# Kernel optimization log

Measured on AMD Instinct MI355X. Metric: run time of the kernel, lower is better.

Reference implementation:

```python
import jax, jax.numpy as jnp
import numpy as np

N_NODES = 100000
N_EDGES = 3200000
D = 256
REPEAT = 2
FACTOR = 0.5


def setup_inputs() -> dict:
    key = jax.random.key(0)
    k1, k2, k3, k4, k5, k6 = jax.random.split(key, 6)
    x = jax.random.normal(k1, (N_NODES, D), dtype=jnp.float32)
    vals = jax.random.uniform(k2, (N_EDGES,), dtype=jnp.float32)
    # Xavier-ish scale for linear weights
    W0 = jax.random.normal(k3, (D, D), dtype=jnp.float32) / np.sqrt(D)
    W1 = jax.random.normal(k4, (D, D), dtype=jnp.float32) / np.sqrt(D)
    rows = jax.random.randint(k5, (N_EDGES,), 0, N_NODES, dtype=jnp.int32)
    cols = jax.random.randint(k6, (N_EDGES,), 0, N_NODES, dtype=jnp.int32)
    return {"x": x, "vals": vals, "W0": W0, "W1": W1, "rows": rows, "cols": cols}


def reference(x, vals, W0, W1, rows, cols):
    # support is sparse [N, N] in COO: support[rows[e], cols[e]] = vals[e]
    def spmm(h):
        # gather source-node features, scale by edge weight, scatter-add to dst
        return jax.ops.segment_sum(vals[:, None] * h[cols], rows,
                                   num_segments=N_NODES)

    h = x
    for W, act in ((W0, jax.nn.relu), (W1, lambda v: v)):
        # _propagate: repeated SpMM with scalar factor
        for _ in range(REPEAT):
            h = spmm(h) * FACTOR
        # linear (no bias) + activation
        h = act(h @ W)
    return h
```

## Files before the change

kernel.cpp:

```cpp
#include <hip/hip_runtime.h>
#include <hip/hip_bf16.h>
#include <hip/hip_fp16.h>

#define N_D 256
#define NBLK 832

typedef __attribute__((ext_vector_type(8))) short bf16x8;
typedef __attribute__((ext_vector_type(4))) float f32x4;

__device__ __forceinline__ unsigned short f2bf(float f) {
  union { float f; unsigned u; } c; c.f = f;
  unsigned u = c.u;
  return (unsigned short)((u + 0x7fffu + ((u >> 16) & 1u)) >> 16);
}
__device__ __forceinline__ float asf(unsigned u) {
  union { unsigned u; float f; } c; c.u = u;
  return c.f;
}
__device__ __forceinline__ int grp_of(int r, unsigned gmagic) {
  int g = (int)(((unsigned long long)(unsigned)r * gmagic) >> 37);
  return min(g, 7);
}

__global__ __launch_bounds__(256) void conv_kernel(
    const float* __restrict__ in, unsigned short* __restrict__ out, int n4) {
  int i = blockIdx.x * 256 + threadIdx.x;
  if (i < n4) {
    float4 v = reinterpret_cast<const float4*>(in)[i];
    ushort4 o;
    o.x = f2bf(v.x); o.y = f2bf(v.y); o.z = f2bf(v.z); o.w = f2bf(v.w);
    reinterpret_cast<ushort4*>(out)[i] = o;
  }
}

__global__ __launch_bounds__(256) void count_kernel(
    const int* __restrict__ rows, int* __restrict__ cnt, int* __restrict__ cntT,
    int n_edges, unsigned gmagic) {
  __shared__ int lcnt[8];
  if (threadIdx.x < 8) lcnt[threadIdx.x] = 0;
  __syncthreads();
  for (int e = blockIdx.x * 256 + threadIdx.x; e < n_edges; e += NBLK * 256) {
    const int r = rows[e];
    atomicAdd(&cnt[r], 1);
    atomicAdd(&lcnt[grp_of(r, gmagic)], 1);
  }
  __syncthreads();
  if (threadIdx.x < 8) cntT[threadIdx.x * NBLK + blockIdx.x] = lcnt[threadIdx.x];
}

__global__ __launch_bounds__(1024) void scan_kernel(
    const int* __restrict__ cnt, int* __restrict__ outA,
    int* __restrict__ outB, int n) {
  __shared__ int wsum[16];
  __shared__ int carry_sh;
  const int tid = threadIdx.x;
  const int lane = tid & 63;
  const int wid = tid >> 6;
  if (tid == 0) carry_sh = 0;
  __syncthreads();
  for (int base = 0; base < n; base += 4096) {
    const int i0 = base + tid * 4;
    int4 v = make_int4(0, 0, 0, 0);
    if (i0 + 3 < n) v = *reinterpret_cast<const int4*>(cnt + i0);
    else {
      if (i0     < n) v.x = cnt[i0];
      if (i0 + 1 < n) v.y = cnt[i0 + 1];
      if (i0 + 2 < n) v.z = cnt[i0 + 2];
    }
    const int s1 = v.x, s2 = s1 + v.y, s3 = s2 + v.z, s4 = s3 + v.w;
    int ws = s4;
#pragma unroll
    for (int off = 1; off < 64; off <<= 1) {
      int o = __shfl_up(ws, off, 64);
      if (lane >= off) ws += o;
    }
    if (lane == 63) wsum[wid] = ws;
    __syncthreads();
    if (wid == 0) {
      int t = (lane < 16) ? wsum[lane] : 0;
#pragma unroll
      for (int off = 1; off < 16; off <<= 1) {
        int o = __shfl_up(t, off, 64);
        if (lane >= off) t += o;
      }
      if (lane < 16) wsum[lane] = t;
    }
    __syncthreads();
    const int carry = carry_sh;
    const int tbase = carry + (wid ? wsum[wid - 1] : 0) + ws - s4;
    if (i0     < n) { outA[i0]     = tbase;      outB[i0]     = tbase; }
    if (i0 + 1 < n) { outA[i0 + 1] = tbase + s1; outB[i0 + 1] = tbase + s1; }
    if (i0 + 2 < n) { outA[i0 + 2] = tbase + s2; outB[i0 + 2] = tbase + s2; }
    if (i0 + 3 < n) { outA[i0 + 3] = tbase + s3; outB[i0 + 3] = tbase + s3; }
    __syncthreads();
    if (tid == 0) carry_sh = carry + wsum[15];
    __syncthreads();
  }
  if (tid == 0) outA[n] = carry_sh;
}

__global__ __launch_bounds__(256) void partition_kernel(
    const int* __restrict__ rows, const int* __restrict__ cols,
    const float* __restrict__ vals, const int* __restrict__ pofsT,
    int2* __restrict__ part, int n_edges, unsigned gmagic) {
  __shared__ int lofs[8];
  if (threadIdx.x < 8) lofs[threadIdx.x] = pofsT[threadIdx.x * NBLK + blockIdx.x];
  __syncthreads();
  for (int e = blockIdx.x * 256 + threadIdx.x; e < n_edges; e += NBLK * 256) {
    const int r = rows[e];
    const int g = grp_of(r, gmagic);
    const int slot = atomicAdd(&lofs[g], 1);
    const unsigned short hb = __half_as_ushort(__float2half_rn(vals[e] * 0.5f));
    int2 rv;
    rv.x = r;
    rv.y = (int)(((unsigned)cols[e] << 15) | ((unsigned)hb >> 1));
    part[slot] = rv;
  }
}

__global__ __launch_bounds__(256) void scatter2_kernel(
    const int2* __restrict__ part, const int* __restrict__ pofsT,
    int* __restrict__ cursor, unsigned* __restrict__ colpack) {
  const int g  = blockIdx.x & 7;
  const int bk = blockIdx.x >> 3;
  const int nb = gridDim.x >> 3;
  const int s0 = pofsT[g * NBLK];
  const int s1 = pofsT[(g + 1) * NBLK];
  for (int i = s0 + bk * 256 + threadIdx.x; i < s1; i += nb * 256) {
    const int2 rv = part[i];
    const int pos = atomicAdd(&cursor[rv.x], 1);
    colpack[pos] = (unsigned)rv.y;
  }
}

__global__ __launch_bounds__(256) void spmm_slice(
    const unsigned short* __restrict__ hin, const int* __restrict__ row_ptr,
    const unsigned* __restrict__ colpack, unsigned short* __restrict__ hout,
    int n_nodes) {
  const int slice = blockIdx.x & 3;
  const int lane = threadIdx.x & 63;
  const int half = lane >> 5;
  const int sub  = lane & 31;
  const int wgid = ((blockIdx.x >> 2) * 256 + threadIdx.x) >> 6;
  const int node = wgid * 2 + half;
  const bool ok = node < n_nodes;
  int start = 0, end = 0;
  if (ok) { start = row_ptr[node]; end = row_ptr[node + 1]; }

  const unsigned* __restrict__ hinw = reinterpret_cast<const unsigned*>(hin);
  const int fofs = slice * 32 + sub;

  float acc0 = 0.f, acc1 = 0.f;

  for (int base = start; base < end; base += 32) {
    const int cnt = min(32, end - base);
    unsigned u = 0;
    if (base + sub < end) u = colpack[base + sub];
    for (int t = 0; t < cnt; t += 8) {
      unsigned hv[8];
      float v[8];
#pragma unroll
      for (int j = 0; j < 8; ++j) {
        const unsigned ue = (unsigned)__shfl((int)u, (half << 5) + t + j, 64);
        const int c = (int)(ue >> 15);
        v[j] = __half2float(__ushort_as_half((unsigned short)((ue & 0x7fffu) << 1)));
        hv[j] = hinw[(size_t)c * 128 + fofs];
      }
#pragma unroll
      for (int j = 0; j < 8; ++j) {
        acc0 += v[j] * asf(hv[j] << 16);
        acc1 += v[j] * asf(hv[j] & 0xffff0000u);
      }
    }
  }
  if (ok) {
    reinterpret_cast<unsigned*>(hout)[(size_t)node * 128 + fofs] =
        (unsigned)f2bf(acc0) | ((unsigned)f2bf(acc1) << 16);
  }
}

__global__ __launch_bounds__(256) void wconv_kernel(
    const float* __restrict__ W, unsigned short* __restrict__ WT) {
  int k = blockIdx.x;
  int n = threadIdx.x;
  WT[(size_t)n * N_D + k] = f2bf(W[(size_t)k * N_D + n]);
}

template <bool RELU, bool OUT_BF16>
__global__ __launch_bounds__(256) void gemm_csr(
    const unsigned short* __restrict__ H, const unsigned short* __restrict__ WT,
    void* __restrict__ C, int M) {
  const int wave = threadIdx.x >> 6;
  const int lane = threadIdx.x & 63;
  const int m = lane & 15;
  const int p = lane >> 4;
  const int row0 = blockIdx.x * 64;
  const int col0 = wave * 64;

  f32x4 acc[4][4];
#pragma unroll
  for (int i = 0; i < 4; ++i)
#pragma unroll
    for (int j = 0; j < 4; ++j) acc[i][j] = (f32x4){0.f, 0.f, 0.f, 0.f};

  for (int k0 = 0; k0 < N_D; k0 += 32) {
    bf16x8 a[4], b[4];
#pragma unroll
    for (int rt = 0; rt < 4; ++rt) {
      const int r = row0 + rt * 16 + m;
      if (r < M) {
        a[rt] = *reinterpret_cast<const bf16x8*>(H + (size_t)r * N_D + k0 + p * 8);
      } else {
        a[rt] = (bf16x8){0, 0, 0, 0, 0, 0, 0, 0};
      }
    }
#pragma unroll
    for (int nt = 0; nt < 4; ++nt) {
      b[nt] = *reinterpret_cast<const bf16x8*>(
          WT + (size_t)(col0 + nt * 16 + m) * N_D + k0 + p * 8);
    }
#pragma unroll
    for (int rt = 0; rt < 4; ++rt)
#pragma unroll
      for (int nt = 0; nt < 4; ++nt)
        acc[rt][nt] = __builtin_amdgcn_mfma_f32_16x16x32_bf16(a[rt], b[nt], acc[rt][nt], 0, 0, 0);
  }

#pragma unroll
  for (int rt = 0; rt < 4; ++rt) {
#pragma unroll
    for (int nt = 0; nt < 4; ++nt) {
      const int col = col0 + nt * 16 + m;
#pragma unroll
      for (int rr = 0; rr < 4; ++rr) {
        const int r = row0 + rt * 16 + p * 4 + rr;
        if (r < M) {
          float v = acc[rt][nt][rr];
          if (RELU) v = fmaxf(v, 0.f);
          if (OUT_BF16)
            ((unsigned short*)C)[(size_t)r * N_D + col] = f2bf(v);
          else
            ((float*)C)[(size_t)r * N_D + col] = v;
        }
      }
    }
  }
}

extern "C" void kernel_launch(void* const* d_in, const int* in_sizes, int n_in,
                              void* d_out, int out_size, void* d_ws, size_t ws_size,
                              hipStream_t stream) {
  const float* x    = (const float*)d_in[0];
  const float* vals = (const float*)d_in[1];
  const float* W0   = (const float*)d_in[2];
  const float* W1   = (const float*)d_in[3];
  const int*   rows = (const int*)d_in[4];
  const int*   cols = (const int*)d_in[5];

  const int n_edges = in_sizes[1];
  const int M = in_sizes[0] / N_D;
  const size_t n_feat = (size_t)M * N_D;

  char* ws = (char*)d_ws;
  unsigned short* hA      = (unsigned short*)(ws);
  unsigned*       colpack = (unsigned*)(ws + 51200000);
  int*            row_ptr = (int*)(ws + 64000000);
  int*            cursor  = (int*)(ws + 64400128);
  int*            cnt     = (int*)(ws + 64800256);
  int*            cntT    = (int*)(ws + 65200384);
  int*            pofsT   = (int*)(ws + 65227264);
  int*            pscr    = (int*)(ws + 65254144);
  unsigned short* wt      = (unsigned short*)(ws + 65281024);
  unsigned short* hB   = (unsigned short*)d_out;
  unsigned short* xb   = (unsigned short*)d_out + n_feat;
  int2*           part = (int2*)((char*)d_out + 51200000);

  const int sblocks = 4 * ((M + 7) / 8);
  const int gblocks = (M + 63) / 64;
  const int cblocks = (int)(n_feat / 4 + 255) / 256;
  const int rpg = (M + 7) / 8;
  const unsigned gmagic = (unsigned)(((1ULL << 37) + rpg - 1) / (unsigned long long)rpg);

  hipMemsetAsync(cnt, 0, (size_t)M * sizeof(int), stream);
  count_kernel<<<NBLK, 256, 0, stream>>>(rows, cnt, cntT, n_edges, gmagic);
  scan_kernel<<<1, 1024, 0, stream>>>(cnt, row_ptr, cursor, M);
  scan_kernel<<<1, 1024, 0, stream>>>(cntT, pofsT, pscr, 8 * NBLK);
  partition_kernel<<<NBLK, 256, 0, stream>>>(rows, cols, vals, pofsT, part,
                                             n_edges, gmagic);
  scatter2_kernel<<<NBLK, 256, 0, stream>>>(part, pofsT, cursor, colpack);
  conv_kernel<<<cblocks, 256, 0, stream>>>(x, xb, (int)(n_feat / 4));

  spmm_slice<<<sblocks, 256, 0, stream>>>(xb, row_ptr, colpack, hA, M);
  spmm_slice<<<sblocks, 256, 0, stream>>>(hA, row_ptr, colpack, hB, M);
  wconv_kernel<<<N_D, N_D, 0, stream>>>(W0, wt);
  gemm_csr<true, true><<<gblocks, 256, 0, stream>>>(hB, wt, hA, M);

  spmm_slice<<<sblocks, 256, 0, stream>>>(hA, row_ptr, colpack, hB, M);
  spmm_slice<<<sblocks, 256, 0, stream>>>(hB, row_ptr, colpack, hA, M);
  wconv_kernel<<<N_D, N_D, 0, stream>>>(W1, wt);
  gemm_csr<false, false><<<gblocks, 256, 0, stream>>>(hA, wt, d_out, M);
}
```

Before: 1.224 ms.

## Privatize row counts, parallelize row-pointer scan, precompute SpMM offsets, retile GEMM

Row-degree counting now goes into 8 private count arrays, one per block group, to reduce atomic contention. The arrays are then summed, and the single-block scan over 100k nodes is replaced by a three-step multi-block scan (block sums, scan of the sums, apply). In the SpMM, each lane decodes its column offset and edge weight once before the shuffles, removing per-element decode work in the inner loop. The GEMM is retiled so each wave covers 16 rows by all 256 columns, reusing one A fragment across 16 MFMAs, at the cost of more accumulator registers and more loads of the weight matrix.

```diff
diff --git a/kernel.cpp b/kernel.cpp
--- a/kernel.cpp
+++ b/kernel.cpp
@@ -34,11 +34,12 @@
 }
 
 __global__ __launch_bounds__(256) void count_kernel(
-    const int* __restrict__ rows, int* __restrict__ cnt, int* __restrict__ cntT,
-    int n_edges, unsigned gmagic) {
+    const int* __restrict__ rows, int* __restrict__ cnt8, int* __restrict__ cntT,
+    int n_edges, unsigned gmagic, int M) {
   __shared__ int lcnt[8];
   if (threadIdx.x < 8) lcnt[threadIdx.x] = 0;
   __syncthreads();
+  int* __restrict__ cnt = cnt8 + (size_t)(blockIdx.x & 7) * M;
   for (int e = blockIdx.x * 256 + threadIdx.x; e < n_edges; e += NBLK * 256) {
     const int r = rows[e];
     atomicAdd(&cnt[r], 1);
@@ -46,6 +47,25 @@
   }
   __syncthreads();
   if (threadIdx.x < 8) cntT[threadIdx.x * NBLK + blockIdx.x] = lcnt[threadIdx.x];
+}
+
+__global__ __launch_bounds__(256) void sumcnt_kernel(
+    const int* __restrict__ cnt8, int* __restrict__ cnts,
+    int* __restrict__ bsum, int M) {
+  __shared__ int wred[4];
+  const int i = blockIdx.x * 256 + threadIdx.x;
+  int s = 0;
+  if (i < M) {
+#pragma unroll
+    for (int k = 0; k < 8; ++k) s += cnt8[(size_t)k * M + i];
+    cnts[i] = s;
+  }
+  int t = s;
+#pragma unroll
+  for (int off = 32; off; off >>= 1) t += __shfl_down(t, off, 64);
+  if ((threadIdx.x & 63) == 0) wred[threadIdx.x >> 6] = t;
+  __syncthreads();
+  if (threadIdx.x == 0) bsum[blockIdx.x] = wred[0] + wred[1] + wred[2] + wred[3];
 }
 
 __global__ __launch_bounds__(1024) void scan_kernel(
@@ -97,6 +117,30 @@
     __syncthreads();
   }
   if (tid == 0) outA[n] = carry_sh;
+}
+
+__global__ __launch_bounds__(256) void scan_apply_kernel(
+    const int* __restrict__ cnts, const int* __restrict__ bofs,
+    int* __restrict__ row_ptr, int* __restrict__ cursor, int M) {
+  __shared__ int wsum[4];
+  const int tid = threadIdx.x;
+  const int lane = tid & 63;
+  const int wid = tid >> 6;
+  const int i = blockIdx.x * 256 + tid;
+  const int v = (i < M) ? cnts[i] : 0;
+  int s = v;
+#pragma unroll
+  for (int off = 1; off < 64; off <<= 1) {
+    int o = __shfl_up(s, off, 64);
+    if (lane >= off) s += o;
+  }
+  if (lane == 63) wsum[wid] = s;
+  __syncthreads();
+  int add = 0;
+  for (int k = 0; k < wid; ++k) add += wsum[k];
+  const int excl = bofs[blockIdx.x] + add + s - v;
+  if (i < M) { row_ptr[i] = excl; cursor[i] = excl; }
+  if (i == M) row_ptr[M] = bofs[gridDim.x];
 }
 
 __global__ __launch_bounds__(256) void partition_kernel(
@@ -149,6 +193,7 @@
 
   const unsigned* __restrict__ hinw = reinterpret_cast<const unsigned*>(hin);
   const int fofs = slice * 32 + sub;
+  const int sbase = half << 5;
 
   float acc0 = 0.f, acc1 = 0.f;
 
@@ -156,15 +201,16 @@
     const int cnt = min(32, end - base);
     unsigned u = 0;
     if (base + sub < end) u = colpack[base + sub];
+    const int opre = (int)((u >> 15) << 7);
+    const float vpre = __half2float(__ushort_as_half((unsigned short)((u & 0x7fffu) << 1)));
     for (int t = 0; t < cnt; t += 8) {
       unsigned hv[8];
       float v[8];
 #pragma unroll
       for (int j = 0; j < 8; ++j) {
-        const unsigned ue = (unsigned)__shfl((int)u, (half << 5) + t + j, 64);
-        const int c = (int)(ue >> 15);
-        v[j] = __half2float(__ushort_as_half((unsigned short)((ue & 0x7fffu) << 1)));
-        hv[j] = hinw[(size_t)c * 128 + fofs];
+        const int oj = __shfl(opre, sbase + t + j, 64);
+        v[j] = __shfl(vpre, sbase + t + j, 64);
+        hv[j] = hinw[(size_t)(unsigned)(oj + fofs)];
       }
 #pragma unroll
       for (int j = 0; j < 8; ++j) {
@@ -187,61 +233,46 @@
 }
 
 template <bool RELU, bool OUT_BF16>
-__global__ __launch_bounds__(256) void gemm_csr(
+__global__ __launch_bounds__(256) void gemm2(
     const unsigned short* __restrict__ H, const unsigned short* __restrict__ WT,
     void* __restrict__ C, int M) {
   const int wave = threadIdx.x >> 6;
   const int lane = threadIdx.x & 63;
   const int m = lane & 15;
   const int p = lane >> 4;
-  const int row0 = blockIdx.x * 64;
-  const int col0 = wave * 64;
-
-  f32x4 acc[4][4];
-#pragma unroll
-  for (int i = 0; i < 4; ++i)
-#pragma unroll
-    for (int j = 0; j < 4; ++j) acc[i][j] = (f32x4){0.f, 0.f, 0.f, 0.f};
+  const int row0 = blockIdx.x * 64 + wave * 16;
+
+  f32x4 acc[16];
+#pragma unroll
+  for (int i = 0; i < 16; ++i) acc[i] = (f32x4){0.f, 0.f, 0.f, 0.f};
+
+  const int r = row0 + m;
+  const bool rok = r < M;
 
   for (int k0 = 0; k0 < N_D; k0 += 32) {
-    bf16x8 a[4], b[4];
-#pragma unroll
-    for (int rt = 0; rt < 4; ++rt) {
-      const int r = row0 + rt * 16 + m;
-      if (r < M) {
-        a[rt] = *reinterpret_cast<const bf16x8*>(H + (size_t)r * N_D + k0 + p * 8);
-      } else {
-        a[rt] = (bf16x8){0, 0, 0, 0, 0, 0, 0, 0};
-      }
-    }
-#pragma unroll
-    for (int nt = 0; nt < 4; ++nt) {
-      b[nt] = *reinterpret_cast<const bf16x8*>(
-          WT + (size_t)(col0 + nt * 16 + m) * N_D + k0 + p * 8);
-    }
-#pragma unroll
-    for (int rt = 0; rt < 4; ++rt)
-#pragma unroll
-      for (int nt = 0; nt < 4; ++nt)
-        acc[rt][nt] = __builtin_amdgcn_mfma_f32_16x16x32_bf16(a[rt], b[nt], acc[rt][nt], 0, 0, 0);
-  }
-
-#pragma unroll
-  for (int rt = 0; rt < 4; ++rt) {
-#pragma unroll
-    for (int nt = 0; nt < 4; ++nt) {
-      const int col = col0 + nt * 16 + m;
-#pragma unroll
-      for (int rr = 0; rr < 4; ++rr) {
-        const int r = row0 + rt * 16 + p * 4 + rr;
-        if (r < M) {
-          float v = acc[rt][nt][rr];
-          if (RELU) v = fmaxf(v, 0.f);
-          if (OUT_BF16)
-            ((unsigned short*)C)[(size_t)r * N_D + col] = f2bf(v);
-          else
-            ((float*)C)[(size_t)r * N_D + col] = v;
-        }
+    bf16x8 a = {0, 0, 0, 0, 0, 0, 0, 0};
+    if (rok) a = *reinterpret_cast<const bf16x8*>(H + (size_t)r * N_D + k0 + p * 8);
+#pragma unroll
+    for (int nt = 0; nt < 16; ++nt) {
+      const bf16x8 b = *reinterpret_cast<const bf16x8*>(
+          WT + (size_t)(nt * 16 + m) * N_D + k0 + p * 8);
+      acc[nt] = __builtin_amdgcn_mfma_f32_16x16x32_bf16(a, b, acc[nt], 0, 0, 0);
+    }
+  }
+
+#pragma unroll
+  for (int nt = 0; nt < 16; ++nt) {
+    const int col = nt * 16 + m;
+#pragma unroll
+    for (int rr = 0; rr < 4; ++rr) {
+      const int r2 = row0 + p * 4 + rr;
+      if (r2 < M) {
+        float vv = acc[nt][rr];
+        if (RELU) vv = fmaxf(vv, 0.f);
+        if (OUT_BF16)
+          ((unsigned short*)C)[(size_t)r2 * N_D + col] = f2bf(vv);
+        else
+          ((float*)C)[(size_t)r2 * N_D + col] = vv;
       }
     }
   }
@@ -266,24 +297,31 @@
   unsigned*       colpack = (unsigned*)(ws + 51200000);
   int*            row_ptr = (int*)(ws + 64000000);
   int*            cursor  = (int*)(ws + 64400128);
-  int*            cnt     = (int*)(ws + 64800256);
-  int*            cntT    = (int*)(ws + 65200384);
-  int*            pofsT   = (int*)(ws + 65227264);
-  int*            pscr    = (int*)(ws + 65254144);
-  unsigned short* wt      = (unsigned short*)(ws + 65281024);
+  int*            cnt8    = (int*)(ws + 64800256);
+  int*            cnts    = (int*)(ws + 68000384);
+  int*            bsum    = (int*)(ws + 68400512);
+  int*            bofs    = (int*)(ws + 68402560);
+  int*            bscr    = (int*)(ws + 68404608);
+  int*            cntT    = (int*)(ws + 68406656);
+  int*            pofsT   = (int*)(ws + 68433536);
+  int*            pscr    = (int*)(ws + 68460416);
+  unsigned short* wt      = (unsigned short*)(ws + 68487296);
   unsigned short* hB   = (unsigned short*)d_out;
   unsigned short* xb   = (unsigned short*)d_out + n_feat;
   int2*           part = (int2*)((char*)d_out + 51200000);
 
+  const int Mb = (M + 255) / 256;
   const int sblocks = 4 * ((M + 7) / 8);
   const int gblocks = (M + 63) / 64;
   const int cblocks = (int)(n_feat / 4 + 255) / 256;
   const int rpg = (M + 7) / 8;
   const unsigned gmagic = (unsigned)(((1ULL << 37) + rpg - 1) / (unsigned long long)rpg);
 
-  hipMemsetAsync(cnt, 0, (size_t)M * sizeof(int), stream);
-  count_kernel<<<NBLK, 256, 0, stream>>>(rows, cnt, cntT, n_edges, gmagic);
-  scan_kernel<<<1, 1024, 0, stream>>>(cnt, row_ptr, cursor, M);
+  hipMemsetAsync(cnt8, 0, (size_t)8 * M * sizeof(int), stream);
+  count_kernel<<<NBLK, 256, 0, stream>>>(rows, cnt8, cntT, n_edges, gmagic, M);
+  sumcnt_kernel<<<Mb, 256, 0, stream>>>(cnt8, cnts, bsum, M);
+  scan_kernel<<<1, 1024, 0, stream>>>(bsum, bofs, bscr, Mb);
+  scan_apply_kernel<<<Mb, 256, 0, stream>>>(cnts, bofs, row_ptr, cursor, M);
   scan_kernel<<<1, 1024, 0, stream>>>(cntT, pofsT, pscr, 8 * NBLK);
   partition_kernel<<<NBLK, 256, 0, stream>>>(rows, cols, vals, pofsT, part,
                                              n_edges, gmagic);
@@ -293,10 +331,10 @@
   spmm_slice<<<sblocks, 256, 0, stream>>>(xb, row_ptr, colpack, hA, M);
   spmm_slice<<<sblocks, 256, 0, stream>>>(hA, row_ptr, colpack, hB, M);
   wconv_kernel<<<N_D, N_D, 0, stream>>>(W0, wt);
-  gemm_csr<true, true><<<gblocks, 256, 0, stream>>>(hB, wt, hA, M);
+  gemm2<true, true><<<gblocks, 256, 0, stream>>>(hB, wt, hA, M);
 
   spmm_slice<<<sblocks, 256, 0, stream>>>(hA, row_ptr, colpack, hB, M);
   spmm_slice<<<sblocks, 256, 0, stream>>>(hB, row_ptr, colpack, hA, M);
   wconv_kernel<<<N_D, N_D, 0, stream>>>(W1, wt);
-  gemm_csr<false, false><<<gblocks, 256, 0, stream>>>(hA, wt, d_out, M);
-}
+  gemm2<false, false><<<gblocks, 256, 0, stream>>>(hA, wt, d_out, M);
+}
```

New measurement: 1.273 ms. 4.0% more time.
